# Performance work log

Hardware: AMD Instinct MI355X
Metric: run time of the kernel (lower is better)

## Reference

```python
import jax, jax.numpy as jnp
import numpy as np

LAMBDA_SOFTMAX = 9.0   # opt.lambda_softmax
LAMBDA_LSE = 6.0       # opt.lambda_lse
MARGIN = 0.2
EPS = 1e-8


def setup_inputs() -> dict:
    key = jax.random.key(0)
    k1, k2, k3, k4 = jax.random.split(key, 4)
    N, F, W, D = 64, 64, 40, 512
    images = jax.random.normal(k1, (N, F, D), dtype=jnp.float32)
    captions = jax.random.normal(k2, (N, W, D), dtype=jnp.float32)
    img_lens = jax.random.randint(k3, (N,), F // 2, F + 1)
    cap_lens = jax.random.randint(k4, (N,), W // 2, W + 1)
    return {"images": images, "captions": captions,
            "img_lens": img_lens, "cap_lens": cap_lens}


def _xattn_scores(images, captions, img_lens, cap_lens):
    # images: (N, F, D) queries; captions: (N, W, D) contexts
    N, F, D = images.shape
    W = captions.shape[1]
    fmask = jnp.arange(F)[None, :] < img_lens[:, None]   # (N_img, F)
    wmask = jnp.arange(W)[None, :] < cap_lens[:, None]   # (N_cap, W)
    # raw attention for every (caption j, image i) pair: (j, i, w, f)
    A = jnp.einsum('jwd,ifd->jiwf', captions, images)
    pair_mask = wmask[:, None, :, None] & fmask[None, :, None, :]
    A = jnp.where(pair_mask, A, 0.0)
    # clipped_l2norm: LeakyReLU(0.1) then l2-normalize along frame axis
    A = jnp.where(A > 0, A, 0.1 * A)
    A = A / (jnp.sqrt(jnp.sum(A * A, axis=3, keepdims=True)) + EPS)
    # softmax over words (sourceL) with temperature lambda_softmax
    logits = jnp.swapaxes(A, 2, 3) * LAMBDA_SOFTMAX       # (j, i, f, w)
    logits = jnp.where(wmask[:, None, None, :], logits, -jnp.inf)
    aw = jax.nn.softmax(logits, axis=-1)                  # (j, i, f, w)
    # weighted context per frame: (j, i, f, d)
    wctx = jnp.einsum('jifw,jwd->jifd', aw, captions)
    # per-frame cosine similarity between image frame and weighted context
    num = jnp.einsum('ifd,jifd->jif', images, wctx)
    n1 = jnp.linalg.norm(images, axis=-1)                 # (i, f)
    n2 = jnp.linalg.norm(wctx, axis=-1)                   # (j, i, f)
    sim = num / jnp.maximum(n1[None, :, :] * n2, EPS)     # (j, i, f)
    # LogSumExp aggregation over valid frames (unstabilized, as in torch)
    e = jnp.exp(sim * LAMBDA_LSE) * fmask[None, :, :]
    scores = jnp.log(jnp.sum(e, axis=-1)) / LAMBDA_LSE    # (n_cap, n_img)
    return scores


def reference(images, captions, img_lens, cap_lens):
    S = _xattn_scores(images, captions, img_lens, cap_lens)  # (N, N)
    diag = jnp.diagonal(S)
    eye = jnp.eye(S.shape[0], dtype=bool)
    cost_s = jnp.maximum(MARGIN + S - diag[:, None], 0.0)
    cost_im = jnp.maximum(MARGIN + S - diag[None, :], 0.0)
    cost_s = jnp.where(eye, 0.0, cost_s)
    cost_im = jnp.where(eye, 0.0, cost_im)
    # max_violation=True: hardest negative per row/col
    return jnp.max(cost_s, axis=1).sum() + jnp.max(cost_im, axis=0).sum()
```

## Files before the change

### kernel.cpp

```cpp
#include <hip/hip_runtime.h>
#include <math.h>

#define N 64
#define F 64
#define W 40
#define D 512
#define LSM 9.0f
#define LLSE 6.0f
#define MARG 0.2f
#define ESTR 56

typedef _Float16 f16x8 __attribute__((ext_vector_type(8)));
typedef _Float16 f16x4 __attribute__((ext_vector_type(4)));
typedef float f32x4 __attribute__((ext_vector_type(4)));

__device__ inline void gll16(const void* g, void* l) {
  __builtin_amdgcn_global_load_lds(
      (const __attribute__((address_space(1))) unsigned int*)g,
      (__attribute__((address_space(3))) unsigned int*)l, 16, 0, 0);
}


__global__ __launch_bounds__(512) void k_pre(
    const float* __restrict__ img, const float* __restrict__ cap,
    _Float16* __restrict__ img_h, _Float16* __restrict__ cap_h,
    _Float16* __restrict__ G_h, float* __restrict__ n1) {
  __shared__ __align__(16) _Float16 capT[4 * 48 * 128];
  int t = threadIdx.x;
  int b = blockIdx.x;
  if (b < 128) {
    int i = b >> 1;
    int f = ((b & 1) << 5) + (t >> 4);
    int q = t & 15;
    const float* row = img + ((size_t)i * F + f) * D + q * 32;
    _Float16* dsti = img_h + (size_t)i * 32768;
    int fsw = (f & 7) << 3;
    float s = 0.f;
#pragma unroll
    for (int k = 0; k < 4; ++k) {
      float4 u = *(const float4*)(row + k * 8);
      float4 v = *(const float4*)(row + k * 8 + 4);
      s += u.x * u.x + u.y * u.y + u.z * u.z + u.w * u.w;
      s += v.x * v.x + v.y * v.y + v.z * v.z + v.w * v.w;
      f16x8 h;
      h[0] = (_Float16)u.x; h[1] = (_Float16)u.y; h[2] = (_Float16)u.z; h[3] = (_Float16)u.w;
      h[4] = (_Float16)v.x; h[5] = (_Float16)v.y; h[6] = (_Float16)v.z; h[7] = (_Float16)v.w;
      int d = q * 32 + k * 8;
      int ch = d >> 6, din = d & 63;
      *(f16x8*)(dsti + ch * 4096 + f * 64 + (din ^ fsw)) = h;
    }
    s += __shfl_xor(s, 1);
    s += __shfl_xor(s, 2);
    s += __shfl_xor(s, 4);
    s += __shfl_xor(s, 8);
    if (q == 0) n1[i * F + f] = sqrtf(s);
  } else {
    int j = b - 128;
    int lane = t & 63, wv = t >> 6;
    const float* src = cap + (size_t)j * W * D;
    _Float16* dst = cap_h + (size_t)j * 24576;
#pragma unroll
    for (int k = 0; k < 6; ++k) {
      int slot = t + k * 512;
      int w = slot >> 6, d = (slot & 63) * 8;
      float4 u = {0.f, 0.f, 0.f, 0.f}, v = {0.f, 0.f, 0.f, 0.f};
      if (w < W) {
        u = *(const float4*)(src + (size_t)w * D + d);
        v = *(const float4*)(src + (size_t)w * D + d + 4);
      }
      f16x8 h;
      h[0] = (_Float16)u.x; h[1] = (_Float16)u.y; h[2] = (_Float16)u.z; h[3] = (_Float16)u.w;
      h[4] = (_Float16)v.x; h[5] = (_Float16)v.y; h[6] = (_Float16)v.z; h[7] = (_Float16)v.w;
      int wsw = (w & 7) << 3;
      int ch2 = d >> 6, din2 = d & 63;
      *(f16x8*)(dst + ch2 * 3072 + w * 64 + (din2 ^ wsw)) = h;
      int chO = d >> 7, dinO = d & 127;
      *(f16x8*)(capT + chO * 6144 + w * 128 + (dinO ^ wsw)) = h;
    }
    __syncthreads();
    int rlo = lane & 15, hi = lane >> 4;
    int koff = hi * 8, sw = (rlo & 7) << 3;
    _Float16* gb = G_h + (size_t)j * 3072;
    for (int tile = wv; tile < 9; tile += 8) {
      int mt = tile / 3, kt = tile % 3;
      f32x4 acc = (f32x4)0.f;
#pragma unroll
      for (int ks = 0; ks < 16; ++ks) {
        int kk = ks * 32 + koff;
        int ch = kk >> 7, din = (kk & 127) ^ sw;
        f16x8 af = *(const f16x8*)(capT + ch * 6144 + (mt * 16 + rlo) * 128 + din);
        f16x8 bf = *(const f16x8*)(capT + ch * 6144 + (kt * 16 + rlo) * 128 + din);
        acc = __builtin_amdgcn_mfma_f32_16x16x32_f16(af, bf, acc, 0, 0, 0);
      }
#pragma unroll
      for (int r = 0; r < 4; ++r) {
        int w = mt * 16 + hi * 4 + r, k = kt * 16 + rlo;
        float val = (w < W && k < W) ? acc[r] : 0.f;
        gb[w * 64 + k] = (_Float16)val;
      }
    }
    if (t < 96) {
      int w = t >> 1, c8 = 48 + (t & 1) * 8;
      *(f16x8*)(gb + w * 64 + c8) = (f16x8)(_Float16)0.f;
    }
  }
}

__device__ inline void stage_chunk(const char* capb, const char* imgb, int ch,
                                   char* dst, int wv, int lane) {
#pragma unroll
  for (int s = 0; s < 5; ++s) {
    int m = s * 8 + wv;
    const char* src;
    if (m < 24) {
      src = capb + (m / 6) * 49152 + ch * 6144 + (m % 6) * 1024;
    } else {
      int e = (m - 24) >> 3;
      src = imgb + e * 65536 + ch * 8192 + ((m - 24) & 7) * 1024;
    }
    gll16(src + lane * 16, dst + m * 1024);
  }
}

__global__ __launch_bounds__(512, 4) void k_main(
    const _Float16* __restrict__ img_h, const _Float16* __restrict__ cap_h,
    const int* __restrict__ imgL, const int* __restrict__ capL,
    const float* __restrict__ n1g, const _Float16* __restrict__ G_h,
    float* __restrict__ S) {
  __shared__ __align__(16) char buf[81920];

  int t = threadIdx.x;
  int lane = t & 63, wv = t >> 6;
  int rlo = lane & 15, hi = lane >> 4;
  int koff = hi * 8;
  int sw = (rlo & 7) << 3;

  int bid = blockIdx.x;
  int xcd = bid & 7, s0 = bid >> 3;
  int it = xcd * 4 + (s0 >> 4);
  int jt = s0 & 15;
  int jloc = wv & 3, iloc = wv >> 2;
  int j = jt * 4 + jloc;
  int i = it * 2 + iloc;

  int iL = imgL[i], cL = capL[j];

  const char* capb = (const char*)cap_h + (size_t)jt * 4 * 49152;
  const char* imgb = (const char*)img_h + (size_t)it * 2 * 65536;

  f32x4 acc[3][4];
#pragma unroll
  for (int mt = 0; mt < 3; ++mt)
#pragma unroll
    for (int nt = 0; nt < 4; ++nt) acc[mt][nt] = (f32x4)0.f;

  stage_chunk(capb, imgb, 0, buf, wv, lane);

#pragma unroll
  for (int c = 0; c < 8; ++c) {
    if (c < 7) stage_chunk(capb, imgb, c + 1, buf + ((c + 1) & 1) * 40960, wv, lane);
    if (c < 7) {
      asm volatile("s_waitcnt vmcnt(5)" ::: "memory");
    } else {
      asm volatile("s_waitcnt vmcnt(0)" ::: "memory");
    }
    __builtin_amdgcn_s_barrier();
    __builtin_amdgcn_sched_barrier(0);
    const char* cb = buf + (c & 1) * 40960;
    const _Float16* myCap = (const _Float16*)cb + jloc * 3072;
    const _Float16* myImg = (const _Float16*)(cb + 24576) + iloc * 4096;
#pragma unroll
    for (int ks = 0; ks < 2; ++ks) {
      int col = (ks * 32 + koff) ^ sw;
      f16x8 af[3], bf[4];
#pragma unroll
      for (int mt = 0; mt < 3; ++mt) af[mt] = *(const f16x8*)(myCap + (mt * 16 + rlo) * 64 + col);
#pragma unroll
      for (int nt = 0; nt < 4; ++nt) bf[nt] = *(const f16x8*)(myImg + (nt * 16 + rlo) * 64 + col);
#pragma unroll
      for (int mt = 0; mt < 3; ++mt)
#pragma unroll
        for (int nt = 0; nt < 4; ++nt)
          acc[mt][nt] = __builtin_amdgcn_mfma_f32_16x16x32_f16(af[mt], bf[nt], acc[mt][nt], 0, 0, 0);
    }
    __builtin_amdgcn_sched_barrier(0);
    __builtin_amdgcn_s_barrier();
  }

  _Float16* Ew = (_Float16*)(buf + wv * 7168);
  float n1lane = n1g[i * F + lane];

  float rinv[3][4];
#pragma unroll
  for (int mt = 0; mt < 3; ++mt)
#pragma unroll
    for (int r = 0; r < 4; ++r) {
      float s = 0.f;
#pragma unroll
      for (int nt = 0; nt < 4; ++nt) {
        float a = acc[mt][nt][r];
        float l = a > 0.f ? a : 0.1f * a;
        s += ((nt * 16 + rlo) < iL) ? l * l : 0.f;
      }
#pragma unroll
      for (int d = 1; d < 16; d <<= 1) s += __shfl_xor(s, d);
      rinv[mt][r] = 1.f / (sqrtf(s) + 1e-8f);
    }

  float sn[4] = {0.f, 0.f, 0.f, 0.f};
#pragma unroll
  for (int mt = 0; mt < 3; ++mt)
#pragma unroll
    for (int nt = 0; nt < 4; ++nt) {
      f16x4 ev;
#pragma unroll
      for (int r = 0; r < 4; ++r) {
        int w = mt * 16 + hi * 4 + r;
        float a = acc[mt][nt][r];
        float l = a > 0.f ? a : 0.1f * a;
        float e = (w < cL) ? __expf(LSM * l * rinv[mt][r]) : 0.f;
        sn[nt] = fmaf(e, a, sn[nt]);
        ev[r] = (_Float16)e;
      }
      *(f16x4*)(Ew + (nt * 16 + rlo) * ESTR + mt * 16 + hi * 4) = ev;
    }
#pragma unroll
  for (int nt = 0; nt < 4; ++nt) {
    sn[nt] += __shfl_xor(sn[nt], 16);
    sn[nt] += __shfl_xor(sn[nt], 32);
  }

  const _Float16* gB = G_h + (size_t)j * 3072 + rlo * 64 + koff;
  f32x4 P[4][3];
#pragma unroll
  for (int mtl = 0; mtl < 4; ++mtl)
#pragma unroll
    for (int ntl = 0; ntl < 3; ++ntl) P[mtl][ntl] = (f32x4)0.f;
#pragma unroll
  for (int ks2 = 0; ks2 < 2; ++ks2) {
    int kk2 = ks2 * 32;
    f16x8 bfg[3];
#pragma unroll
    for (int ntl = 0; ntl < 3; ++ntl) bfg[ntl] = *(const f16x8*)(gB + ntl * 1024 + kk2);
#pragma unroll
    for (int mtl = 0; mtl < 4; ++mtl) {
      f16x8 af = *(const f16x8*)(Ew + (mtl * 16 + rlo) * ESTR + kk2 + koff);
#pragma unroll
      for (int ntl = 0; ntl < 3; ++ntl)
        P[mtl][ntl] = __builtin_amdgcn_mfma_f32_16x16x32_f16(af, bfg[ntl], P[mtl][ntl], 0, 0, 0);
    }
  }

  float ef = 0.f;
#pragma unroll
  for (int mtl = 0; mtl < 4; ++mtl) {
#pragma unroll
    for (int rr = 0; rr < 4; ++rr) {
      int fm = mtl * 16 + hi * 4 + rr;
      float n2s = 0.f;
#pragma unroll
      for (int ntl = 0; ntl < 3; ++ntl) {
        float evv = (float)Ew[fm * ESTR + ntl * 16 + rlo];
        n2s = fmaf(P[mtl][ntl][rr], evv, n2s);
      }
#pragma unroll
      for (int d = 1; d < 16; d <<= 1) n2s += __shfl_xor(n2s, d);
      float nm = __shfl(sn[mtl], hi * 4 + rr);
      float n1v = __shfl(n1lane, fm);
      float denom = n1v * sqrtf(fmaxf(n2s, 0.f));
      float sim = nm / fmaxf(denom, 1e-20f);
      ef += (fm < iL) ? __expf(LLSE * sim) : 0.f;
    }
  }
  ef += __shfl_xor(ef, 16);
  ef += __shfl_xor(ef, 32);
  if (lane == 0) S[(j << 6) + i] = __logf(ef) * (1.f / LLSE);
}

__global__ void k_loss(const float* __restrict__ S, float* __restrict__ out) {
  __shared__ float red[128];
  int t = threadIdx.x;
  float m = -1e30f;
  if (t < 64) {
    int a = t;
    float da = S[a * N + a];
    for (int b = 0; b < N; ++b)
      if (b != a) m = fmaxf(m, MARG + S[a * N + b] - da);
  } else {
    int b = t - 64;
    float db = S[b * N + b];
    for (int a = 0; a < N; ++a)
      if (a != b) m = fmaxf(m, MARG + S[a * N + b] - db);
  }
  m = fmaxf(m, 0.f);
  red[t] = m;
  __syncthreads();
  if (t == 0) {
    float s = 0.f;
    for (int k = 0; k < 128; ++k) s += red[k];
    *out = s;
  }
}

extern "C" void kernel_launch(void* const* d_in, const int* in_sizes, int n_in,
                              void* d_out, int out_size, void* d_ws, size_t ws_size,
                              hipStream_t stream) {
  const float* img = (const float*)d_in[0];
  const float* cap = (const float*)d_in[1];
  const int* imgL = (const int*)d_in[2];
  const int* capL = (const int*)d_in[3];

  char* wsb = (char*)d_ws;
  float* n1 = (float*)wsb;
  float* S = (float*)(wsb + 16384);
  _Float16* img_h = (_Float16*)(wsb + 32768);
  _Float16* cap_h = (_Float16*)(wsb + 32768 + 4194304);
  _Float16* G_h = (_Float16*)(wsb + 32768 + 4194304 + 3145728);

  k_pre<<<192, 512, 0, stream>>>(img, cap, img_h, cap_h, G_h, n1);
  k_main<<<512, 512, 0, stream>>>(img_h, cap_h, imgL, capL, n1, G_h, S);
  k_loss<<<1, 128, 0, stream>>>(S, (float*)d_out);
}
```

Measured before the change: 56.81 us.

## Split image conversion across more blocks, remap main tiles, precompute staging addresses

The image fp16 conversion in the prep kernel now uses 256 blocks with 32 threads per frame instead of 128 blocks with 16, which raises parallelism for the memory-bound conversion. The main kernel remaps block indices so each XCD covers a 16x32 (i,j) quadrant, aiming at better L2 reuse of shared image and caption tiles. Per-wave global-to-LDS source addresses are precomputed once and only offset by the chunk stride, which removes repeated address arithmetic. The loss kernel replaces its serial 128-element sum with a wavefront shuffle reduction.

```diff
diff --git a/kernel.cpp b/kernel.cpp
--- a/kernel.cpp
+++ b/kernel.cpp
@@ -28,16 +28,18 @@
   __shared__ __align__(16) _Float16 capT[4 * 48 * 128];
   int t = threadIdx.x;
   int b = blockIdx.x;
-  if (b < 128) {
-    int i = b >> 1;
-    int f = ((b & 1) << 5) + (t >> 4);
-    int q = t & 15;
-    const float* row = img + ((size_t)i * F + f) * D + q * 32;
+  if (b < 256) {
+    int i = b >> 2;
+    int f = ((b & 3) << 4) + (t >> 5);
+    int q = t & 31;
+    const float* row = img + ((size_t)i * F + f) * D + q * 16;
     _Float16* dsti = img_h + (size_t)i * 32768;
     int fsw = (f & 7) << 3;
     float s = 0.f;
-#pragma unroll
-    for (int k = 0; k < 4; ++k) {
+    int d0 = q * 16;
+    int ch = d0 >> 6, din = d0 & 63;
+#pragma unroll
+    for (int k = 0; k < 2; ++k) {
       float4 u = *(const float4*)(row + k * 8);
       float4 v = *(const float4*)(row + k * 8 + 4);
       s += u.x * u.x + u.y * u.y + u.z * u.z + u.w * u.w;
@@ -45,17 +47,16 @@
       f16x8 h;
       h[0] = (_Float16)u.x; h[1] = (_Float16)u.y; h[2] = (_Float16)u.z; h[3] = (_Float16)u.w;
       h[4] = (_Float16)v.x; h[5] = (_Float16)v.y; h[6] = (_Float16)v.z; h[7] = (_Float16)v.w;
-      int d = q * 32 + k * 8;
-      int ch = d >> 6, din = d & 63;
-      *(f16x8*)(dsti + ch * 4096 + f * 64 + (din ^ fsw)) = h;
+      *(f16x8*)(dsti + ch * 4096 + f * 64 + ((din + k * 8) ^ fsw)) = h;
     }
     s += __shfl_xor(s, 1);
     s += __shfl_xor(s, 2);
     s += __shfl_xor(s, 4);
     s += __shfl_xor(s, 8);
+    s += __shfl_xor(s, 16);
     if (q == 0) n1[i * F + f] = sqrtf(s);
   } else {
-    int j = b - 128;
+    int j = b - 256;
     int lane = t & 63, wv = t >> 6;
     const float* src = cap + (size_t)j * W * D;
     _Float16* dst = cap_h + (size_t)j * 24576;
@@ -106,22 +107,6 @@
   }
 }
 
-__device__ inline void stage_chunk(const char* capb, const char* imgb, int ch,
-                                   char* dst, int wv, int lane) {
-#pragma unroll
-  for (int s = 0; s < 5; ++s) {
-    int m = s * 8 + wv;
-    const char* src;
-    if (m < 24) {
-      src = capb + (m / 6) * 49152 + ch * 6144 + (m % 6) * 1024;
-    } else {
-      int e = (m - 24) >> 3;
-      src = imgb + e * 65536 + ch * 8192 + ((m - 24) & 7) * 1024;
-    }
-    gll16(src + lane * 16, dst + m * 1024);
-  }
-}
-
 __global__ __launch_bounds__(512, 4) void k_main(
     const _Float16* __restrict__ img_h, const _Float16* __restrict__ cap_h,
     const int* __restrict__ imgL, const int* __restrict__ capL,
@@ -137,16 +122,30 @@
 
   int bid = blockIdx.x;
   int xcd = bid & 7, s0 = bid >> 3;
-  int it = xcd * 4 + (s0 >> 4);
-  int jt = s0 & 15;
   int jloc = wv & 3, iloc = wv >> 2;
-  int j = jt * 4 + jloc;
-  int i = it * 2 + iloc;
+  int i = (xcd & 3) * 16 + (s0 & 7) * 2 + iloc;
+  int j = (xcd >> 2) * 32 + (s0 >> 3) * 4 + jloc;
 
   int iL = imgL[i], cL = capL[j];
 
-  const char* capb = (const char*)cap_h + (size_t)jt * 4 * 49152;
-  const char* imgb = (const char*)img_h + (size_t)it * 2 * 65536;
+  const char* capb = (const char*)cap_h + (size_t)(j - jloc) * 49152;
+  const char* imgb = (const char*)img_h + (size_t)(i - iloc) * 65536;
+
+  const char* bsrc[5];
+  int cstr[5], mdst[5];
+#pragma unroll
+  for (int s = 0; s < 5; ++s) {
+    int m = s * 8 + wv;
+    if (m < 24) {
+      bsrc[s] = capb + (m / 6) * 49152 + (m % 6) * 1024 + lane * 16;
+      cstr[s] = 6144;
+    } else {
+      int e = m - 24;
+      bsrc[s] = imgb + (e >> 3) * 65536 + (e & 7) * 1024 + lane * 16;
+      cstr[s] = 8192;
+    }
+    mdst[s] = m * 1024;
+  }
 
   f32x4 acc[3][4];
 #pragma unroll
@@ -154,12 +153,15 @@
 #pragma unroll
     for (int nt = 0; nt < 4; ++nt) acc[mt][nt] = (f32x4)0.f;
 
-  stage_chunk(capb, imgb, 0, buf, wv, lane);
+#pragma unroll
+  for (int s = 0; s < 5; ++s) gll16(bsrc[s], buf + mdst[s]);
 
 #pragma unroll
   for (int c = 0; c < 8; ++c) {
-    if (c < 7) stage_chunk(capb, imgb, c + 1, buf + ((c + 1) & 1) * 40960, wv, lane);
     if (c < 7) {
+      char* db = buf + ((c + 1) & 1) * 40960;
+#pragma unroll
+      for (int s = 0; s < 5; ++s) gll16(bsrc[s] + (c + 1) * cstr[s], db + mdst[s]);
       asm volatile("s_waitcnt vmcnt(5)" ::: "memory");
     } else {
       asm volatile("s_waitcnt vmcnt(0)" ::: "memory");
@@ -292,13 +294,13 @@
     for (int a = 0; a < N; ++a)
       if (a != b) m = fmaxf(m, MARG + S[a * N + b] - db);
   }
-  m = fmaxf(m, 0.f);
-  red[t] = m;
+  red[t] = fmaxf(m, 0.f);
   __syncthreads();
-  if (t == 0) {
-    float s = 0.f;
-    for (int k = 0; k < 128; ++k) s += red[k];
-    *out = s;
+  if (t < 64) {
+    float v = red[t] + red[t + 64];
+#pragma unroll
+    for (int off = 1; off < 64; off <<= 1) v += __shfl_xor(v, off);
+    if (t == 0) *out = v;
   }
 }
 
@@ -317,7 +319,7 @@
   _Float16* cap_h = (_Float16*)(wsb + 32768 + 4194304);
   _Float16* G_h = (_Float16*)(wsb + 32768 + 4194304 + 3145728);
 
-  k_pre<<<192, 512, 0, stream>>>(img, cap, img_h, cap_h, G_h, n1);
+  k_pre<<<320, 512, 0, stream>>>(img, cap, img_h, cap_h, G_h, n1);
   k_main<<<512, 512, 0, stream>>>(img_h, cap_h, imgL, capL, n1, G_h, S);
   k_loss<<<1, 128, 0, stream>>>(S, (float*)d_out);
 }
```

Result: no change. 56.74 us (-0.1%).
